# Optimization experiments

Measured on AMD Instinct MI355X. Metric: run time of the kernel, lower is better.

Reference implementation:

```python
import jax, jax.numpy as jnp
import numpy as np

NUM_HEADS = 4
D_MODEL = 192
NEG_INF = -1000000000.0  # fp32 branch of the original mask fill


def setup_inputs() -> dict:
    key = jax.random.key(0)
    ks = jax.random.split(key, 9)
    b, s, d = 4, 2048, D_MODEL
    inp = {
        "query": jax.random.normal(ks[0], (b, s, d), dtype=jnp.float32),
        "key": jax.random.normal(ks[1], (b, s, d), dtype=jnp.float32),
        "value": jax.random.normal(ks[2], (b, s, d), dtype=jnp.float32),
        "attn_mask": jax.random.randint(ks[3], (b, s, s), 0, 2, dtype=jnp.int32),
        "bias": jax.random.normal(ks[4], (1, NUM_HEADS, s, s), dtype=jnp.float32) * 0.1,
        # nn.Linear(d, d, bias=False) weights, applied as x @ W.T
        "Wq": jax.random.normal(ks[5], (d, d), dtype=jnp.float32) / np.sqrt(d),
        "Wk": jax.random.normal(ks[6], (d, d), dtype=jnp.float32) / np.sqrt(d),
        "Wv": jax.random.normal(ks[7], (d, d), dtype=jnp.float32) / np.sqrt(d),
        "Wo": jax.random.normal(ks[8], (d, d), dtype=jnp.float32) / np.sqrt(d),
    }
    return inp


def reference(query, key, value, attn_mask, bias, Wq, Wk, Wv, Wo):
    b, s, d = query.shape
    h, dh = NUM_HEADS, d // NUM_HEADS
    # QKV projections (Linear, no bias): x @ W.T
    q = (query @ Wq.T).reshape(b, s, h, dh)   # [b,s,h,dh]
    k = (key @ Wk.T).reshape(b, s, h, dh)
    v = (value @ Wv.T).reshape(b, s, h, dh)
    # unscaled dot-product logits (original has no 1/sqrt(d) scaling)
    logits = jnp.einsum("bqhd,bkhd->bhqk", q, k)
    logits = logits + bias                       # bias added BEFORE mask fill
    mask4 = attn_mask[:, None, :, :]             # [b,1,q,k] -> broadcast over heads
    logits = jnp.where(mask4 == 0, NEG_INF, logits)
    weights = jax.nn.softmax(logits, axis=-1)    # [b,h,q,k]
    # dropout_rate=0.0 (eval-mode / identity dropout)
    out = jnp.einsum("bhqk,bkhd->bqhd", weights, v).reshape(b, s, d)
    out = out @ Wo.T
    return out, weights.mean(axis=1)             # ([b,s,d], [b,s,s])
```

## Files before the change

kernel.cpp:

```cpp
#include <hip/hip_runtime.h>

#define BB 4
#define SS 2048
#define HH 4
#define DD 192
#define QT 16
#define NT (SS / 2 / 64)
#define NEG_BIG (-1e9f)
#define MB_NEG 0xCE6Eu

typedef __attribute__((ext_vector_type(8))) short short8;
typedef __attribute__((ext_vector_type(4))) float f32x4;

__device__ inline ushort f2bf(float x) {
    union { float f; unsigned u; } v; v.f = x;
    unsigned r = (v.u + 0x7FFFu + ((v.u >> 16) & 1u)) >> 16;
    return (ushort)r;
}
__device__ inline float bf2f(ushort x) {
    union { unsigned u; float f; } v; v.u = ((unsigned)x) << 16;
    return v.f;
}
__device__ inline void wave_lds_fence() {
    __builtin_amdgcn_wave_barrier();
    __builtin_amdgcn_s_waitcnt(0xC07F);
    __builtin_amdgcn_wave_barrier();
}

__global__ __launch_bounds__(256) void wt_kernel(
    const float* __restrict__ Wq, const float* __restrict__ Wk,
    const float* __restrict__ Wv, const float* __restrict__ Wo,
    float* __restrict__ WTall)
{
    __shared__ float tile[32][33];
    const float* W = (blockIdx.z == 0) ? Wq : (blockIdx.z == 1) ? Wk
                   : (blockIdx.z == 2) ? Wv : Wo;
    float* WT = WTall + (size_t)blockIdx.z * DD * DD;
    const int c0 = blockIdx.x * 32, j0 = blockIdx.y * 32;
    const int tx = threadIdx.x & 31, ty = threadIdx.x >> 5;
#pragma unroll
    for (int k = 0; k < 4; ++k)
        tile[ty + 8 * k][tx] = W[(size_t)(j0 + ty + 8 * k) * DD + c0 + tx];
    __syncthreads();
#pragma unroll
    for (int k = 0; k < 4; ++k)
        WT[(size_t)(c0 + ty + 8 * k) * DD + j0 + tx] = tile[tx][ty + 8 * k];
}

__global__ __launch_bounds__(192) void qkv_proj_kernel(
    const float* __restrict__ Xq, const float* __restrict__ Xk,
    const float* __restrict__ Xv, const float* __restrict__ WTall,
    ushort* __restrict__ qpad, ushort* __restrict__ kpad,
    ushort* __restrict__ vT)
{
    const int mode = blockIdx.y;
    const float* __restrict__ X = (mode == 0) ? Xq : (mode == 1) ? Xk : Xv;
    const float* __restrict__ WT = WTall + (size_t)mode * DD * DD;

    __shared__ __align__(16) float xs[16][DD];
    const int row0 = blockIdx.x * 16;
    const int t = threadIdx.x;
    {
        const float4* src = (const float4*)(X + (size_t)row0 * DD);
        float4* dst = (float4*)&xs[0][0];
        for (int i = t; i < 16 * DD / 4; i += 192) dst[i] = src[i];
    }
    __syncthreads();

    const int jt = (t % 48) * 4;
    const int rowg = t / 48;

    float acc[4][4];
#pragma unroll
    for (int r = 0; r < 4; ++r)
#pragma unroll
        for (int j = 0; j < 4; ++j) acc[r][j] = 0.f;

#pragma unroll 2
    for (int k4 = 0; k4 < DD / 4; ++k4) {
        float4 w0 = *(const float4*)&WT[(size_t)(k4 * 4 + 0) * DD + jt];
        float4 w1 = *(const float4*)&WT[(size_t)(k4 * 4 + 1) * DD + jt];
        float4 w2 = *(const float4*)&WT[(size_t)(k4 * 4 + 2) * DD + jt];
        float4 w3 = *(const float4*)&WT[(size_t)(k4 * 4 + 3) * DD + jt];
#pragma unroll
        for (int r = 0; r < 4; ++r) {
            float4 xv = *(const float4*)&xs[rowg * 4 + r][k4 * 4];
            acc[r][0] = fmaf(xv.x, w0.x, acc[r][0]); acc[r][1] = fmaf(xv.x, w0.y, acc[r][1]);
            acc[r][2] = fmaf(xv.x, w0.z, acc[r][2]); acc[r][3] = fmaf(xv.x, w0.w, acc[r][3]);
            acc[r][0] = fmaf(xv.y, w1.x, acc[r][0]); acc[r][1] = fmaf(xv.y, w1.y, acc[r][1]);
            acc[r][2] = fmaf(xv.y, w1.z, acc[r][2]); acc[r][3] = fmaf(xv.y, w1.w, acc[r][3]);
            acc[r][0] = fmaf(xv.z, w2.x, acc[r][0]); acc[r][1] = fmaf(xv.z, w2.y, acc[r][1]);
            acc[r][2] = fmaf(xv.z, w2.z, acc[r][2]); acc[r][3] = fmaf(xv.z, w2.w, acc[r][3]);
            acc[r][0] = fmaf(xv.w, w3.x, acc[r][0]); acc[r][1] = fmaf(xv.w, w3.y, acc[r][1]);
            acc[r][2] = fmaf(xv.w, w3.z, acc[r][2]); acc[r][3] = fmaf(xv.w, w3.w, acc[r][3]);
        }
    }

    if (mode < 2) {
        ushort* __restrict__ out = (mode == 0) ? qpad : kpad;
        const int hd = jt / 48, f = jt % 48;
#pragma unroll
        for (int r = 0; r < 4; ++r) {
            ushort4 o;
            o.x = f2bf(acc[r][0]); o.y = f2bf(acc[r][1]);
            o.z = f2bf(acc[r][2]); o.w = f2bf(acc[r][3]);
            *(ushort4*)&out[((size_t)(row0 + rowg * 4 + r) * HH + hd) * 64 + f] = o;
        }
        const int4 z = make_int4(0, 0, 0, 0);
        for (int i = t; i < 128; i += 192) {
            const int row = i >> 3, hh = (i >> 1) & 3, half = i & 1;
            *(int4*)&out[((size_t)(row0 + row) * HH + hh) * 64 + 48 + half * 8] = z;
        }
    } else {
        const int b = row0 >> 11, s0 = row0 & (SS - 1);
#pragma unroll
        for (int j = 0; j < 4; ++j) {
            const int col = jt + j, hd = col / 48, f = col % 48;
#pragma unroll
            for (int p = 0; p < 2; ++p) {
                unsigned pk = (unsigned)f2bf(acc[2 * p][j]) |
                              ((unsigned)f2bf(acc[2 * p + 1][j]) << 16);
                *(unsigned*)&vT[(((size_t)b * HH + hd) * 48 + f) * SS +
                                s0 + rowg * 4 + 2 * p] = pk;
            }
        }
    }
}

__global__ __launch_bounds__(192) void o_proj_kernel(
    const float* __restrict__ X, const float* __restrict__ WT,
    float* __restrict__ Y)
{
    __shared__ __align__(16) float xs[16][DD];
    const int row0 = blockIdx.x * 16;
    const int t = threadIdx.x;
    {
        const float4* src = (const float4*)(X + (size_t)row0 * DD);
        float4* dst = (float4*)&xs[0][0];
        for (int i = t; i < 16 * DD / 4; i += 192) dst[i] = src[i];
    }
    __syncthreads();

    const int jt = (t % 48) * 4;
    const int rowg = t / 48;

    float acc[4][4];
#pragma unroll
    for (int r = 0; r < 4; ++r)
#pragma unroll
        for (int j = 0; j < 4; ++j) acc[r][j] = 0.f;

#pragma unroll 2
    for (int k4 = 0; k4 < DD / 4; ++k4) {
        float4 w0 = *(const float4*)&WT[(size_t)(k4 * 4 + 0) * DD + jt];
        float4 w1 = *(const float4*)&WT[(size_t)(k4 * 4 + 1) * DD + jt];
        float4 w2 = *(const float4*)&WT[(size_t)(k4 * 4 + 2) * DD + jt];
        float4 w3 = *(const float4*)&WT[(size_t)(k4 * 4 + 3) * DD + jt];
#pragma unroll
        for (int r = 0; r < 4; ++r) {
            float4 xv = *(const float4*)&xs[rowg * 4 + r][k4 * 4];
            acc[r][0] = fmaf(xv.x, w0.x, acc[r][0]); acc[r][1] = fmaf(xv.x, w0.y, acc[r][1]);
            acc[r][2] = fmaf(xv.x, w0.z, acc[r][2]); acc[r][3] = fmaf(xv.x, w0.w, acc[r][3]);
            acc[r][0] = fmaf(xv.y, w1.x, acc[r][0]); acc[r][1] = fmaf(xv.y, w1.y, acc[r][1]);
            acc[r][2] = fmaf(xv.y, w1.z, acc[r][2]); acc[r][3] = fmaf(xv.y, w1.w, acc[r][3]);
            acc[r][0] = fmaf(xv.z, w2.x, acc[r][0]); acc[r][1] = fmaf(xv.z, w2.y, acc[r][1]);
            acc[r][2] = fmaf(xv.z, w2.z, acc[r][2]); acc[r][3] = fmaf(xv.z, w2.w, acc[r][3]);
            acc[r][0] = fmaf(xv.w, w3.x, acc[r][0]); acc[r][1] = fmaf(xv.w, w3.y, acc[r][1]);
            acc[r][2] = fmaf(xv.w, w3.z, acc[r][2]); acc[r][3] = fmaf(xv.w, w3.w, acc[r][3]);
        }
    }

#pragma unroll
    for (int r = 0; r < 4; ++r)
        *(float4*)&Y[(size_t)(row0 + rowg * 4 + r) * DD + jt] =
            make_float4(acc[r][0], acc[r][1], acc[r][2], acc[r][3]);
}

__device__ inline f32x4 qk_tile(const ushort* kp, short8 qa0, short8 qa1) {
    short8 kb0 = *(const short8*)(kp);
    short8 kb1 = *(const short8*)(kp + 32);
    f32x4 d = {0.f, 0.f, 0.f, 0.f};
    d = __builtin_amdgcn_mfma_f32_16x16x32_bf16(qa0, kb0, d, 0, 0, 0);
    d = __builtin_amdgcn_mfma_f32_16x16x32_bf16(qa1, kb1, d, 0, 0, 0);
    return d;
}

__global__ __launch_bounds__(512, 4) void attn_kernel(
    const ushort* __restrict__ qpad, const ushort* __restrict__ kpad,
    const ushort* __restrict__ vT, const int* __restrict__ mask,
    const float* __restrict__ bias,
    ushort* __restrict__ wscr, float* __restrict__ linv_g,
    float* __restrict__ oattn)
{
    __shared__ __align__(16) ushort wb[8][QT][72];
    __shared__ float l_scr[8][QT];

    const int b  = blockIdx.x >> 7;
    const int q0 = (blockIdx.x & 127) * QT;
    const int t = threadIdx.x;
    const int w = t >> 6;
    const int h = w & 3;
    const int kh = w >> 2;
    const int lane = t & 63;
    const int n16 = lane & 15, quad = lane >> 4;
    const int kbase0 = kh * (SS / 2);

    const ushort* qbase =
        qpad + ((size_t)(b * SS + q0 + n16) * HH + h) * 64 + quad * 8;
    const short8 qa0 = *(const short8*)(qbase);
    const short8 qa1 = *(const short8*)(qbase + 32);
    const ushort* kbase = kpad + (size_t)b * SS * HH * 64 + h * 64 + quad * 8;

    const int srow = lane >> 4;
    const int skey = (lane & 15) * 4;
    const int* mrow0 = mask + (size_t)(b * SS + q0) * SS + kbase0 + skey;
    const float* brow0 = bias + (size_t)(h * SS + q0) * SS + kbase0 + skey;

    float l_[4] = {0.f, 0.f, 0.f, 0.f};
    f32x4 pv[3];
#pragma unroll
    for (int nb = 0; nb < 3; ++nb) pv[nb] = (f32x4){0.f, 0.f, 0.f, 0.f};

    int4  mzc[4];
    float4 bvc[4];
#pragma unroll
    for (int rr = 0; rr < 4; ++rr) {
        const int row = rr * 4 + srow;
        mzc[rr] = *(const int4*)(mrow0 + (size_t)row * SS);
        bvc[rr] = *(const float4*)(brow0 + (size_t)row * SS);
    }

    for (int kt = 0; kt < NT; ++kt) {
        const int kb = kt * 64;
#pragma unroll
        for (int rr = 0; rr < 4; ++rr) {
            const int row = rr * 4 + srow;
            ushort4 o;
            o.x = mzc[rr].x ? f2bf(bvc[rr].x) : (ushort)MB_NEG;
            o.y = mzc[rr].y ? f2bf(bvc[rr].y) : (ushort)MB_NEG;
            o.z = mzc[rr].z ? f2bf(bvc[rr].z) : (ushort)MB_NEG;
            o.w = mzc[rr].w ? f2bf(bvc[rr].w) : (ushort)MB_NEG;
            *(ushort4*)&wb[w][row][skey] = o;
        }
        if (kt + 1 < NT) {
#pragma unroll
            for (int rr = 0; rr < 4; ++rr) {
                const int row = rr * 4 + srow;
                mzc[rr] = *(const int4*)(mrow0 + (size_t)row * SS + kb + 64);
                bvc[rr] = *(const float4*)(brow0 + (size_t)row * SS + kb + 64);
            }
        }
        wave_lds_fence();

#pragma unroll
        for (int g = 0; g < 4; ++g) {
            const int key = kbase0 + kb + g * 16 + n16;
            f32x4 d = qk_tile(kbase + (size_t)key * (HH * 64), qa0, qa1);
#pragma unroll
            for (int r = 0; r < 4; ++r) {
                float wgt = __expf(d[r] + bf2f(wb[w][quad * 4 + r][g * 16 + n16]));
                l_[r] += wgt;
                wb[w][quad * 4 + r][g * 16 + n16] = f2bf(wgt);
            }
        }
        wave_lds_fence();

        const short8 wa0 = *(const short8*)&wb[w][n16][quad * 8];
        const short8 wa1 = *(const short8*)&wb[w][n16][32 + quad * 8];
#pragma unroll
        for (int nb = 0; nb < 3; ++nb) {
            const ushort* vb = vT + ((size_t)(b * HH + h) * 48 + nb * 16 + n16) * SS
                               + kbase0 + kb + quad * 8;
            short8 v0 = *(const short8*)(vb);
            short8 v1 = *(const short8*)(vb + 32);
            pv[nb] = __builtin_amdgcn_mfma_f32_16x16x32_bf16(wa0, v0, pv[nb], 0, 0, 0);
            pv[nb] = __builtin_amdgcn_mfma_f32_16x16x32_bf16(wa1, v1, pv[nb], 0, 0, 0);
        }

        {
            const int r4 = lane >> 4;
            const int k4 = (lane & 15) * 4;
#pragma unroll
            for (int it = 0; it < 4; ++it) {
                const int row = it * 4 + r4;
                ushort4 wv = *(const ushort4*)&wb[w][row][k4];
                *(ushort4*)&wscr[((size_t)(b * SS + q0 + row) * HH + h) * SS +
                                 kbase0 + kb + k4] = wv;
            }
        }
        wave_lds_fence();
    }

#pragma unroll
    for (int r = 0; r < 4; ++r) {
        float ll = l_[r];
#pragma unroll
        for (int off = 1; off < 16; off <<= 1) ll += __shfl_xor(ll, off);
        l_[r] = ll;
    }
    if (n16 == 0) {
#pragma unroll
        for (int r = 0; r < 4; ++r) l_scr[w][quad * 4 + r] = l_[r];
    }

    __syncthreads();

    float* scr = (float*)&wb[0][0][0];
    if (kh == 1) {
#pragma unroll
        for (int nb = 0; nb < 3; ++nb)
            *(f32x4*)&scr[((size_t)(h * 64 + lane)) * 12 + nb * 4] = pv[nb];
    }
    __syncthreads();

    if (kh == 0) {
        float linv[4];
#pragma unroll
        for (int r = 0; r < 4; ++r)
            linv[r] = 1.0f / (l_scr[h][quad * 4 + r] + l_scr[h + 4][quad * 4 + r]);
        if (n16 == 0) {
#pragma unroll
            for (int r = 0; r < 4; ++r)
                linv_g[((size_t)b * HH + h) * SS + q0 + quad * 4 + r] = linv[r];
        }
#pragma unroll
        for (int nb = 0; nb < 3; ++nb) {
            f32x4 po = *(const f32x4*)&scr[((size_t)(h * 64 + lane)) * 12 + nb * 4];
#pragma unroll
            for (int r = 0; r < 4; ++r)
                oattn[((size_t)(b * SS + q0 + quad * 4 + r)) * DD +
                      h * 48 + nb * 16 + n16] = (pv[nb][r] + po[r]) * linv[r];
        }
    }
}

__global__ __launch_bounds__(256) void out1_kernel(
    const ushort* __restrict__ wscr, const float* __restrict__ linv_g,
    float* __restrict__ out1)
{
    const int bq = blockIdx.x;
    const int b = bq >> 11;
    const int q = bq & (SS - 1);
    const int t = threadIdx.x;
    const ushort* base = wscr + (size_t)bq * (HH * SS) + t * 8;

    float li[HH];
#pragma unroll
    for (int hh = 0; hh < HH; ++hh)
        li[hh] = linv_g[((size_t)b * HH + hh) * SS + q] * 0.25f;

    float acc[8];
#pragma unroll
    for (int j = 0; j < 8; ++j) acc[j] = 0.f;

#pragma unroll
    for (int hh = 0; hh < HH; ++hh) {
        short8 wv = *(const short8*)(base + (size_t)hh * SS);
#pragma unroll
        for (int j = 0; j < 8; ++j)
            acc[j] = fmaf(bf2f((ushort)wv[j]), li[hh], acc[j]);
    }

    float* dst = out1 + (size_t)bq * SS + t * 8;
    *(float4*)dst = make_float4(acc[0], acc[1], acc[2], acc[3]);
    *(float4*)(dst + 4) = make_float4(acc[4], acc[5], acc[6], acc[7]);
}

extern "C" void kernel_launch(void* const* d_in, const int* in_sizes, int n_in,
                              void* d_out, int out_size, void* d_ws, size_t ws_size,
                              hipStream_t stream)
{
    const float* query = (const float*)d_in[0];
    const float* key   = (const float*)d_in[1];
    const float* value = (const float*)d_in[2];
    const int*   amask = (const int*)d_in[3];
    const float* bias  = (const float*)d_in[4];
    const float* Wq    = (const float*)d_in[5];
    const float* Wk    = (const float*)d_in[6];
    const float* Wv    = (const float*)d_in[7];
    const float* Wo    = (const float*)d_in[8];

    const size_t n_rows = (size_t)BB * SS;
    float* out0 = (float*)d_out;
    float* out1 = out0 + n_rows * DD;

    ushort* qpad  = (ushort*)d_ws;
    ushort* kpad  = qpad + n_rows * HH * 64;
    ushort* vT    = kpad + n_rows * HH * 64;
    float*  oattn = (float*)(vT + (size_t)BB * HH * 48 * SS);
    float*  WTall = oattn + n_rows * DD;
    float*  linvg = WTall + 4 * DD * DD;
    ushort* wscr  = (ushort*)(linvg + (size_t)BB * HH * SS);

    wt_kernel<<<dim3(6, 6, 4), 256, 0, stream>>>(Wq, Wk, Wv, Wo, WTall);

    qkv_proj_kernel<<<dim3(n_rows / 16, 3), 192, 0, stream>>>(
        query, key, value, WTall, qpad, kpad, vT);

    attn_kernel<<<dim3(BB * SS / QT), 512, 0, stream>>>(
        qpad, kpad, vT, amask, bias, wscr, linvg, oattn);

    out1_kernel<<<dim3(BB * SS), 256, 0, stream>>>(wscr, linvg, out1);

    o_proj_kernel<<<dim3(n_rows / 16), 192, 0, stream>>>(
        oattn, WTall + 3 * DD * DD, out0);
}
```

Baseline: 391.0 us.

## Compute transposed QK tiles so softmax weights feed PV MFMA from registers

The QK MFMA now runs with K as the A operand, which makes each lane own one query row and four consecutive keys. Mask and bias can then be read straight into registers in that layout and applied in fp32, replacing the bf16 mask-bias staging through LDS. The exp'd weights are packed into bf16 registers and used directly as the B operand of the PV MFMA, with V read as split 4-element loads. One LDS round trip and one wave fence per tile are removed, but register pressure rises, so the launch-bounds occupancy hint drops from 4 to 2.

```diff
diff --git a/kernel.cpp b/kernel.cpp
--- a/kernel.cpp
+++ b/kernel.cpp
@@ -7,9 +7,9 @@
 #define QT 16
 #define NT (SS / 2 / 64)
 #define NEG_BIG (-1e9f)
-#define MB_NEG 0xCE6Eu
 
 typedef __attribute__((ext_vector_type(8))) short short8;
+typedef __attribute__((ext_vector_type(4))) short s16x4;
 typedef __attribute__((ext_vector_type(4))) float f32x4;
 
 __device__ inline ushort f2bf(float x) {
@@ -176,16 +176,7 @@
             make_float4(acc[r][0], acc[r][1], acc[r][2], acc[r][3]);
 }
 
-__device__ inline f32x4 qk_tile(const ushort* kp, short8 qa0, short8 qa1) {
-    short8 kb0 = *(const short8*)(kp);
-    short8 kb1 = *(const short8*)(kp + 32);
-    f32x4 d = {0.f, 0.f, 0.f, 0.f};
-    d = __builtin_amdgcn_mfma_f32_16x16x32_bf16(qa0, kb0, d, 0, 0, 0);
-    d = __builtin_amdgcn_mfma_f32_16x16x32_bf16(qa1, kb1, d, 0, 0, 0);
-    return d;
-}
-
-__global__ __launch_bounds__(512, 4) void attn_kernel(
+__global__ __launch_bounds__(512, 2) void attn_kernel(
     const ushort* __restrict__ qpad, const ushort* __restrict__ kpad,
     const ushort* __restrict__ vT, const int* __restrict__ mask,
     const float* __restrict__ bias,
@@ -211,72 +202,82 @@
     const short8 qa1 = *(const short8*)(qbase + 32);
     const ushort* kbase = kpad + (size_t)b * SS * HH * 64 + h * 64 + quad * 8;
 
-    const int srow = lane >> 4;
-    const int skey = (lane & 15) * 4;
-    const int* mrow0 = mask + (size_t)(b * SS + q0) * SS + kbase0 + skey;
-    const float* brow0 = bias + (size_t)(h * SS + q0) * SS + kbase0 + skey;
-
-    float l_[4] = {0.f, 0.f, 0.f, 0.f};
+    const int*   mrow = mask + (size_t)(b * SS + q0 + n16) * SS + kbase0 + quad * 4;
+    const float* brow = bias + (size_t)(h * SS + q0 + n16) * SS + kbase0 + quad * 4;
+    const ushort* vrow = vT + ((size_t)(b * HH + h) * 48 + n16) * SS + kbase0 + quad * 4;
+
+    float l_ = 0.f;
     f32x4 pv[3];
 #pragma unroll
     for (int nb = 0; nb < 3; ++nb) pv[nb] = (f32x4){0.f, 0.f, 0.f, 0.f};
 
-    int4  mzc[4];
+    int4   mzc[4];
     float4 bvc[4];
 #pragma unroll
-    for (int rr = 0; rr < 4; ++rr) {
-        const int row = rr * 4 + srow;
-        mzc[rr] = *(const int4*)(mrow0 + (size_t)row * SS);
-        bvc[rr] = *(const float4*)(brow0 + (size_t)row * SS);
+    for (int g = 0; g < 4; ++g) {
+        mzc[g] = *(const int4*)(mrow + g * 16);
+        bvc[g] = *(const float4*)(brow + g * 16);
     }
 
     for (int kt = 0; kt < NT; ++kt) {
         const int kb = kt * 64;
-#pragma unroll
-        for (int rr = 0; rr < 4; ++rr) {
-            const int row = rr * 4 + srow;
-            ushort4 o;
-            o.x = mzc[rr].x ? f2bf(bvc[rr].x) : (ushort)MB_NEG;
-            o.y = mzc[rr].y ? f2bf(bvc[rr].y) : (ushort)MB_NEG;
-            o.z = mzc[rr].z ? f2bf(bvc[rr].z) : (ushort)MB_NEG;
-            o.w = mzc[rr].w ? f2bf(bvc[rr].w) : (ushort)MB_NEG;
-            *(ushort4*)&wb[w][row][skey] = o;
-        }
+
+        short8 kf[8];
+#pragma unroll
+        for (int g = 0; g < 4; ++g) {
+            const ushort* kp = kbase + (size_t)(kbase0 + kb + g * 16 + n16) * (HH * 64);
+            kf[2 * g]     = *(const short8*)(kp);
+            kf[2 * g + 1] = *(const short8*)(kp + 32);
+        }
+        f32x4 d[4];
+#pragma unroll
+        for (int g = 0; g < 4; ++g) {
+            f32x4 acc = {0.f, 0.f, 0.f, 0.f};
+            acc = __builtin_amdgcn_mfma_f32_16x16x32_bf16(kf[2 * g],     qa0, acc, 0, 0, 0);
+            acc = __builtin_amdgcn_mfma_f32_16x16x32_bf16(kf[2 * g + 1], qa1, acc, 0, 0, 0);
+            d[g] = acc;
+        }
+
+        unsigned wpk[8];
+#pragma unroll
+        for (int g = 0; g < 4; ++g) {
+            float w0 = __expf(d[g][0] + (mzc[g].x ? bvc[g].x : NEG_BIG));
+            float w1 = __expf(d[g][1] + (mzc[g].y ? bvc[g].y : NEG_BIG));
+            float w2 = __expf(d[g][2] + (mzc[g].z ? bvc[g].z : NEG_BIG));
+            float w3 = __expf(d[g][3] + (mzc[g].w ? bvc[g].w : NEG_BIG));
+            l_ += (w0 + w1) + (w2 + w3);
+            unsigned p0 = (unsigned)f2bf(w0) | ((unsigned)f2bf(w1) << 16);
+            unsigned p1 = (unsigned)f2bf(w2) | ((unsigned)f2bf(w3) << 16);
+            wpk[2 * g]     = p0;
+            wpk[2 * g + 1] = p1;
+            *(uint2*)&wb[w][n16][g * 16 + quad * 4] = make_uint2(p0, p1);
+        }
+
         if (kt + 1 < NT) {
 #pragma unroll
-            for (int rr = 0; rr < 4; ++rr) {
-                const int row = rr * 4 + srow;
-                mzc[rr] = *(const int4*)(mrow0 + (size_t)row * SS + kb + 64);
-                bvc[rr] = *(const float4*)(brow0 + (size_t)row * SS + kb + 64);
+            for (int g = 0; g < 4; ++g) {
+                mzc[g] = *(const int4*)(mrow + kb + 64 + g * 16);
+                bvc[g] = *(const float4*)(brow + kb + 64 + g * 16);
             }
         }
+
+#pragma unroll
+        for (int gp = 0; gp < 2; ++gp) {
+            union { unsigned u[4]; short8 s8; } wu;
+            wu.u[0] = wpk[4 * gp + 0]; wu.u[1] = wpk[4 * gp + 1];
+            wu.u[2] = wpk[4 * gp + 2]; wu.u[3] = wpk[4 * gp + 3];
+            const short8 wf8 = wu.s8;
+#pragma unroll
+            for (int nb = 0; nb < 3; ++nb) {
+                const ushort* vp = vrow + (size_t)nb * 16 * SS + kb + gp * 32;
+                s16x4 va = *(const s16x4*)(vp);
+                s16x4 vb = *(const s16x4*)(vp + 16);
+                short8 vf8 = __builtin_shufflevector(va, vb, 0, 1, 2, 3, 4, 5, 6, 7);
+                pv[nb] = __builtin_amdgcn_mfma_f32_16x16x32_bf16(vf8, wf8, pv[nb], 0, 0, 0);
+            }
+        }
+
         wave_lds_fence();
-
-#pragma unroll
-        for (int g = 0; g < 4; ++g) {
-            const int key = kbase0 + kb + g * 16 + n16;
-            f32x4 d = qk_tile(kbase + (size_t)key * (HH * 64), qa0, qa1);
-#pragma unroll
-            for (int r = 0; r < 4; ++r) {
-                float wgt = __expf(d[r] + bf2f(wb[w][quad * 4 + r][g * 16 + n16]));
-                l_[r] += wgt;
-                wb[w][quad * 4 + r][g * 16 + n16] = f2bf(wgt);
-            }
-        }
-        wave_lds_fence();
-
-        const short8 wa0 = *(const short8*)&wb[w][n16][quad * 8];
-        const short8 wa1 = *(const short8*)&wb[w][n16][32 + quad * 8];
-#pragma unroll
-        for (int nb = 0; nb < 3; ++nb) {
-            const ushort* vb = vT + ((size_t)(b * HH + h) * 48 + nb * 16 + n16) * SS
-                               + kbase0 + kb + quad * 8;
-            short8 v0 = *(const short8*)(vb);
-            short8 v1 = *(const short8*)(vb + 32);
-            pv[nb] = __builtin_amdgcn_mfma_f32_16x16x32_bf16(wa0, v0, pv[nb], 0, 0, 0);
-            pv[nb] = __builtin_amdgcn_mfma_f32_16x16x32_bf16(wa1, v1, pv[nb], 0, 0, 0);
-        }
-
         {
             const int r4 = lane >> 4;
             const int k4 = (lane & 15) * 4;
@@ -291,17 +292,9 @@
         wave_lds_fence();
     }
 
-#pragma unroll
-    for (int r = 0; r < 4; ++r) {
-        float ll = l_[r];
-#pragma unroll
-        for (int off = 1; off < 16; off <<= 1) ll += __shfl_xor(ll, off);
-        l_[r] = ll;
-    }
-    if (n16 == 0) {
-#pragma unroll
-        for (int r = 0; r < 4; ++r) l_scr[w][quad * 4 + r] = l_[r];
-    }
+    l_ += __shfl_xor(l_, 16);
+    l_ += __shfl_xor(l_, 32);
+    if (quad == 0) l_scr[w][n16] = l_;
 
     __syncthreads();
 
@@ -314,22 +307,16 @@
     __syncthreads();
 
     if (kh == 0) {
-        float linv[4];
-#pragma unroll
-        for (int r = 0; r < 4; ++r)
-            linv[r] = 1.0f / (l_scr[h][quad * 4 + r] + l_scr[h + 4][quad * 4 + r]);
-        if (n16 == 0) {
-#pragma unroll
-            for (int r = 0; r < 4; ++r)
-                linv_g[((size_t)b * HH + h) * SS + q0 + quad * 4 + r] = linv[r];
-        }
+        const float linv = 1.0f / (l_scr[h][n16] + l_scr[h + 4][n16]);
+        if (quad == 0)
+            linv_g[((size_t)b * HH + h) * SS + q0 + n16] = linv;
 #pragma unroll
         for (int nb = 0; nb < 3; ++nb) {
             f32x4 po = *(const f32x4*)&scr[((size_t)(h * 64 + lane)) * 12 + nb * 4];
 #pragma unroll
             for (int r = 0; r < 4; ++r)
-                oattn[((size_t)(b * SS + q0 + quad * 4 + r)) * DD +
-                      h * 48 + nb * 16 + n16] = (pv[nb][r] + po[r]) * linv[r];
+                oattn[(size_t)(b * SS + q0 + n16) * DD +
+                      h * 48 + nb * 16 + quad * 4 + r] = (pv[nb][r] + po[r]) * linv;
         }
     }
 }
```

Result: slower. 452.9 us (+15.9%).

## Fuse head-mean weights output into attention kernel and double-buffer LDS tiles

Applied to the files above, without the earlier changes.

Folds the separate out1 kernel into the end of the attention kernel. Each block rereads its own just-written bf16 weight rows from global scratch after a threadfence and block barrier, scales them by per-head inverse sums taken from shared memory, and writes the head-averaged weights. Mask and bias are now loaded straight into registers in MFMA output layout, replacing the staging pass through LDS with its bf16 round trip. The LDS weight tile is double-buffered so one wave fence per iteration can go. This saves a kernel launch and the global linv buffer, but the block's epilogue gets longer and per-thread register use rises.

```diff
diff --git a/kernel.cpp b/kernel.cpp
--- a/kernel.cpp
+++ b/kernel.cpp
@@ -7,7 +7,6 @@
 #define QT 16
 #define NT (SS / 2 / 64)
 #define NEG_BIG (-1e9f)
-#define MB_NEG 0xCE6Eu
 
 typedef __attribute__((ext_vector_type(8))) short short8;
 typedef __attribute__((ext_vector_type(4))) float f32x4;
@@ -189,10 +188,10 @@
     const ushort* __restrict__ qpad, const ushort* __restrict__ kpad,
     const ushort* __restrict__ vT, const int* __restrict__ mask,
     const float* __restrict__ bias,
-    ushort* __restrict__ wscr, float* __restrict__ linv_g,
-    float* __restrict__ oattn)
-{
-    __shared__ __align__(16) ushort wb[8][QT][72];
+    ushort* __restrict__ wscr, float* __restrict__ oattn,
+    float* __restrict__ out1)
+{
+    __shared__ __align__(16) ushort wb[2][8][QT][72];
     __shared__ float l_scr[8][QT];
 
     const int b  = blockIdx.x >> 7;
@@ -211,46 +210,27 @@
     const short8 qa1 = *(const short8*)(qbase + 32);
     const ushort* kbase = kpad + (size_t)b * SS * HH * 64 + h * 64 + quad * 8;
 
-    const int srow = lane >> 4;
-    const int skey = (lane & 15) * 4;
-    const int* mrow0 = mask + (size_t)(b * SS + q0) * SS + kbase0 + skey;
-    const float* brow0 = bias + (size_t)(h * SS + q0) * SS + kbase0 + skey;
+    const int*   mq = mask + (size_t)(b * SS + q0 + quad * 4) * SS + kbase0 + n16;
+    const float* bq = bias + (size_t)(h * SS + q0 + quad * 4) * SS + kbase0 + n16;
 
     float l_[4] = {0.f, 0.f, 0.f, 0.f};
     f32x4 pv[3];
 #pragma unroll
     for (int nb = 0; nb < 3; ++nb) pv[nb] = (f32x4){0.f, 0.f, 0.f, 0.f};
 
-    int4  mzc[4];
-    float4 bvc[4];
-#pragma unroll
-    for (int rr = 0; rr < 4; ++rr) {
-        const int row = rr * 4 + srow;
-        mzc[rr] = *(const int4*)(mrow0 + (size_t)row * SS);
-        bvc[rr] = *(const float4*)(brow0 + (size_t)row * SS);
-    }
-
+    int   mz[4][4];
+    float bz[4][4];
+#pragma unroll
+    for (int r = 0; r < 4; ++r)
+#pragma unroll
+        for (int g = 0; g < 4; ++g) {
+            mz[r][g] = mq[(size_t)r * SS + g * 16];
+            bz[r][g] = bq[(size_t)r * SS + g * 16];
+        }
+
+    int buf = 0;
     for (int kt = 0; kt < NT; ++kt) {
         const int kb = kt * 64;
-#pragma unroll
-        for (int rr = 0; rr < 4; ++rr) {
-            const int row = rr * 4 + srow;
-            ushort4 o;
-            o.x = mzc[rr].x ? f2bf(bvc[rr].x) : (ushort)MB_NEG;
-            o.y = mzc[rr].y ? f2bf(bvc[rr].y) : (ushort)MB_NEG;
-            o.z = mzc[rr].z ? f2bf(bvc[rr].z) : (ushort)MB_NEG;
-            o.w = mzc[rr].w ? f2bf(bvc[rr].w) : (ushort)MB_NEG;
-            *(ushort4*)&wb[w][row][skey] = o;
-        }
-        if (kt + 1 < NT) {
-#pragma unroll
-            for (int rr = 0; rr < 4; ++rr) {
-                const int row = rr * 4 + srow;
-                mzc[rr] = *(const int4*)(mrow0 + (size_t)row * SS + kb + 64);
-                bvc[rr] = *(const float4*)(brow0 + (size_t)row * SS + kb + 64);
-            }
-        }
-        wave_lds_fence();
 
 #pragma unroll
         for (int g = 0; g < 4; ++g) {
@@ -258,15 +238,26 @@
             f32x4 d = qk_tile(kbase + (size_t)key * (HH * 64), qa0, qa1);
 #pragma unroll
             for (int r = 0; r < 4; ++r) {
-                float wgt = __expf(d[r] + bf2f(wb[w][quad * 4 + r][g * 16 + n16]));
+                float wgt = __expf(d[r] + (mz[r][g] ? bz[r][g] : NEG_BIG));
                 l_[r] += wgt;
-                wb[w][quad * 4 + r][g * 16 + n16] = f2bf(wgt);
+                wb[buf][w][quad * 4 + r][g * 16 + n16] = f2bf(wgt);
             }
         }
+
+        if (kt + 1 < NT) {
+#pragma unroll
+            for (int r = 0; r < 4; ++r)
+#pragma unroll
+                for (int g = 0; g < 4; ++g) {
+                    mz[r][g] = mq[(size_t)r * SS + kb + 64 + g * 16];
+                    bz[r][g] = bq[(size_t)r * SS + kb + 64 + g * 16];
+                }
+        }
+
         wave_lds_fence();
 
-        const short8 wa0 = *(const short8*)&wb[w][n16][quad * 8];
-        const short8 wa1 = *(const short8*)&wb[w][n16][32 + quad * 8];
+        const short8 wa0 = *(const short8*)&wb[buf][w][n16][quad * 8];
+        const short8 wa1 = *(const short8*)&wb[buf][w][n16][32 + quad * 8];
 #pragma unroll
         for (int nb = 0; nb < 3; ++nb) {
             const ushort* vb = vT + ((size_t)(b * HH + h) * 48 + nb * 16 + n16) * SS
@@ -283,12 +274,12 @@
 #pragma unroll
             for (int it = 0; it < 4; ++it) {
                 const int row = it * 4 + r4;
-                ushort4 wv = *(const ushort4*)&wb[w][row][k4];
+                ushort4 wv = *(const ushort4*)&wb[buf][w][row][k4];
                 *(ushort4*)&wscr[((size_t)(b * SS + q0 + row) * HH + h) * SS +
                                  kbase0 + kb + k4] = wv;
             }
         }
-        wave_lds_fence();
+        buf ^= 1;
     }
 
 #pragma unroll
@@ -303,9 +294,10 @@
         for (int r = 0; r < 4; ++r) l_scr[w][quad * 4 + r] = l_[r];
     }
 
-    __syncthreads();
-
-    float* scr = (float*)&wb[0][0][0];
+    __threadfence();
+    __syncthreads();
+
+    float* scr = (float*)&wb[0][0][0][0];
     if (kh == 1) {
 #pragma unroll
         for (int nb = 0; nb < 3; ++nb)
@@ -318,11 +310,6 @@
 #pragma unroll
         for (int r = 0; r < 4; ++r)
             linv[r] = 1.0f / (l_scr[h][quad * 4 + r] + l_scr[h + 4][quad * 4 + r]);
-        if (n16 == 0) {
-#pragma unroll
-            for (int r = 0; r < 4; ++r)
-                linv_g[((size_t)b * HH + h) * SS + q0 + quad * 4 + r] = linv[r];
-        }
 #pragma unroll
         for (int nb = 0; nb < 3; ++nb) {
             f32x4 po = *(const f32x4*)&scr[((size_t)(h * 64 + lane)) * 12 + nb * 4];
@@ -332,38 +319,32 @@
                       h * 48 + nb * 16 + n16] = (pv[nb][r] + po[r]) * linv[r];
         }
     }
-}
-
-__global__ __launch_bounds__(256) void out1_kernel(
-    const ushort* __restrict__ wscr, const float* __restrict__ linv_g,
-    float* __restrict__ out1)
-{
-    const int bq = blockIdx.x;
-    const int b = bq >> 11;
-    const int q = bq & (SS - 1);
-    const int t = threadIdx.x;
-    const ushort* base = wscr + (size_t)bq * (HH * SS) + t * 8;
-
-    float li[HH];
-#pragma unroll
-    for (int hh = 0; hh < HH; ++hh)
-        li[hh] = linv_g[((size_t)b * HH + hh) * SS + q] * 0.25f;
-
-    float acc[8];
-#pragma unroll
-    for (int j = 0; j < 8; ++j) acc[j] = 0.f;
-
-#pragma unroll
-    for (int hh = 0; hh < HH; ++hh) {
-        short8 wv = *(const short8*)(base + (size_t)hh * SS);
-#pragma unroll
-        for (int j = 0; j < 8; ++j)
-            acc[j] = fmaf(bf2f((ushort)wv[j]), li[hh], acc[j]);
-    }
-
-    float* dst = out1 + (size_t)bq * SS + t * 8;
-    *(float4*)dst = make_float4(acc[0], acc[1], acc[2], acc[3]);
-    *(float4*)(dst + 4) = make_float4(acc[4], acc[5], acc[6], acc[7]);
+
+    {
+        const int row = t >> 5;
+        const int k0 = (t & 31) * 64;
+        float li[HH];
+#pragma unroll
+        for (int hh = 0; hh < HH; ++hh)
+            li[hh] = 0.25f / (l_scr[hh][row] + l_scr[hh + 4][row]);
+        const ushort* wrow = wscr + ((size_t)(b * SS + q0 + row) * HH) * SS + k0;
+        float* orow = out1 + (size_t)(b * SS + q0 + row) * SS + k0;
+#pragma unroll 2
+        for (int c = 0; c < 8; ++c) {
+            float acc[8];
+#pragma unroll
+            for (int j = 0; j < 8; ++j) acc[j] = 0.f;
+#pragma unroll
+            for (int hh = 0; hh < HH; ++hh) {
+                short8 wv = *(const short8*)(wrow + (size_t)hh * SS + c * 8);
+#pragma unroll
+                for (int j = 0; j < 8; ++j)
+                    acc[j] = fmaf(bf2f((ushort)wv[j]), li[hh], acc[j]);
+            }
+            *(float4*)(orow + c * 8) = make_float4(acc[0], acc[1], acc[2], acc[3]);
+            *(float4*)(orow + c * 8 + 4) = make_float4(acc[4], acc[5], acc[6], acc[7]);
+        }
+    }
 }
 
 extern "C" void kernel_launch(void* const* d_in, const int* in_sizes, int n_in,
@@ -389,8 +370,7 @@
     ushort* vT    = kpad + n_rows * HH * 64;
     float*  oattn = (float*)(vT + (size_t)BB * HH * 48 * SS);
     float*  WTall = oattn + n_rows * DD;
-    float*  linvg = WTall + 4 * DD * DD;
-    ushort* wscr  = (ushort*)(linvg + (size_t)BB * HH * SS);
+    ushort* wscr  = (ushort*)(WTall + 4 * DD * DD);
 
     wt_kernel<<<dim3(6, 6, 4), 256, 0, stream>>>(Wq, Wk, Wv, Wo, WTall);
 
@@ -398,9 +378,7 @@
         query, key, value, WTall, qpad, kpad, vT);
 
     attn_kernel<<<dim3(BB * SS / QT), 512, 0, stream>>>(
-        qpad, kpad, vT, amask, bias, wscr, linvg, oattn);
-
-    out1_kernel<<<dim3(BB * SS), 256, 0, stream>>>(wscr, linvg, out1);
+        qpad, kpad, vT, amask, bias, wscr, oattn, out1);
 
     o_proj_kernel<<<dim3(n_rows / 16), 192, 0, stream>>>(
         oattn, WTall + 3 * DD * DD, out0);
```

Measured after the change: 598.3 us. +53.0%, slower.

## Double-buffer mask/bias LDS tile to prefetch next tile during PV

Applied to the files above, without the earlier changes.

Splits the per-wave LDS weight buffer into two halves. While the current tile's softmax weights feed the PV MFMAs and the scratch write, the next tile's mask/bias is converted and staged into the other half, and global loads move two tiles ahead. The goal is to hide mask/bias conversion and global load latency behind the matrix work and drop one fence per iteration. In exchange the block uses twice the LDS for this buffer and holds prefetched registers longer, which may lower occupancy.

```diff
diff --git a/kernel.cpp b/kernel.cpp
--- a/kernel.cpp
+++ b/kernel.cpp
@@ -192,7 +192,7 @@
     ushort* __restrict__ wscr, float* __restrict__ linv_g,
     float* __restrict__ oattn)
 {
-    __shared__ __align__(16) ushort wb[8][QT][72];
+    __shared__ __align__(16) ushort wb[2][8][QT][72];
     __shared__ float l_scr[8][QT];
 
     const int b  = blockIdx.x >> 7;
@@ -229,28 +229,27 @@
         mzc[rr] = *(const int4*)(mrow0 + (size_t)row * SS);
         bvc[rr] = *(const float4*)(brow0 + (size_t)row * SS);
     }
-
+#pragma unroll
+    for (int rr = 0; rr < 4; ++rr) {
+        const int row = rr * 4 + srow;
+        ushort4 o;
+        o.x = mzc[rr].x ? f2bf(bvc[rr].x) : (ushort)MB_NEG;
+        o.y = mzc[rr].y ? f2bf(bvc[rr].y) : (ushort)MB_NEG;
+        o.z = mzc[rr].z ? f2bf(bvc[rr].z) : (ushort)MB_NEG;
+        o.w = mzc[rr].w ? f2bf(bvc[rr].w) : (ushort)MB_NEG;
+        *(ushort4*)&wb[0][w][row][skey] = o;
+    }
+#pragma unroll
+    for (int rr = 0; rr < 4; ++rr) {
+        const int row = rr * 4 + srow;
+        mzc[rr] = *(const int4*)(mrow0 + (size_t)row * SS + 64);
+        bvc[rr] = *(const float4*)(brow0 + (size_t)row * SS + 64);
+    }
+    wave_lds_fence();
+
+    int buf = 0;
     for (int kt = 0; kt < NT; ++kt) {
         const int kb = kt * 64;
-#pragma unroll
-        for (int rr = 0; rr < 4; ++rr) {
-            const int row = rr * 4 + srow;
-            ushort4 o;
-            o.x = mzc[rr].x ? f2bf(bvc[rr].x) : (ushort)MB_NEG;
-            o.y = mzc[rr].y ? f2bf(bvc[rr].y) : (ushort)MB_NEG;
-            o.z = mzc[rr].z ? f2bf(bvc[rr].z) : (ushort)MB_NEG;
-            o.w = mzc[rr].w ? f2bf(bvc[rr].w) : (ushort)MB_NEG;
-            *(ushort4*)&wb[w][row][skey] = o;
-        }
-        if (kt + 1 < NT) {
-#pragma unroll
-            for (int rr = 0; rr < 4; ++rr) {
-                const int row = rr * 4 + srow;
-                mzc[rr] = *(const int4*)(mrow0 + (size_t)row * SS + kb + 64);
-                bvc[rr] = *(const float4*)(brow0 + (size_t)row * SS + kb + 64);
-            }
-        }
-        wave_lds_fence();
 
 #pragma unroll
         for (int g = 0; g < 4; ++g) {
@@ -258,15 +257,37 @@
             f32x4 d = qk_tile(kbase + (size_t)key * (HH * 64), qa0, qa1);
 #pragma unroll
             for (int r = 0; r < 4; ++r) {
-                float wgt = __expf(d[r] + bf2f(wb[w][quad * 4 + r][g * 16 + n16]));
+                float wgt = __expf(d[r] + bf2f(wb[buf][w][quad * 4 + r][g * 16 + n16]));
                 l_[r] += wgt;
-                wb[w][quad * 4 + r][g * 16 + n16] = f2bf(wgt);
+                wb[buf][w][quad * 4 + r][g * 16 + n16] = f2bf(wgt);
             }
         }
+
         wave_lds_fence();
 
-        const short8 wa0 = *(const short8*)&wb[w][n16][quad * 8];
-        const short8 wa1 = *(const short8*)&wb[w][n16][32 + quad * 8];
+        if (kt + 1 < NT) {
+#pragma unroll
+            for (int rr = 0; rr < 4; ++rr) {
+                const int row = rr * 4 + srow;
+                ushort4 o;
+                o.x = mzc[rr].x ? f2bf(bvc[rr].x) : (ushort)MB_NEG;
+                o.y = mzc[rr].y ? f2bf(bvc[rr].y) : (ushort)MB_NEG;
+                o.z = mzc[rr].z ? f2bf(bvc[rr].z) : (ushort)MB_NEG;
+                o.w = mzc[rr].w ? f2bf(bvc[rr].w) : (ushort)MB_NEG;
+                *(ushort4*)&wb[buf ^ 1][w][row][skey] = o;
+            }
+        }
+        if (kt + 2 < NT) {
+#pragma unroll
+            for (int rr = 0; rr < 4; ++rr) {
+                const int row = rr * 4 + srow;
+                mzc[rr] = *(const int4*)(mrow0 + (size_t)row * SS + kb + 128);
+                bvc[rr] = *(const float4*)(brow0 + (size_t)row * SS + kb + 128);
+            }
+        }
+
+        const short8 wa0 = *(const short8*)&wb[buf][w][n16][quad * 8];
+        const short8 wa1 = *(const short8*)&wb[buf][w][n16][32 + quad * 8];
 #pragma unroll
         for (int nb = 0; nb < 3; ++nb) {
             const ushort* vb = vT + ((size_t)(b * HH + h) * 48 + nb * 16 + n16) * SS
@@ -283,12 +304,14 @@
 #pragma unroll
             for (int it = 0; it < 4; ++it) {
                 const int row = it * 4 + r4;
-                ushort4 wv = *(const ushort4*)&wb[w][row][k4];
+                ushort4 wv = *(const ushort4*)&wb[buf][w][row][k4];
                 *(ushort4*)&wscr[((size_t)(b * SS + q0 + row) * HH + h) * SS +
                                  kbase0 + kb + k4] = wv;
             }
         }
+
         wave_lds_fence();
+        buf ^= 1;
     }
 
 #pragma unroll
@@ -305,7 +328,7 @@
 
     __syncthreads();
 
-    float* scr = (float*)&wb[0][0][0];
+    float* scr = (float*)&wb[0][0][0][0];
     if (kh == 1) {
 #pragma unroll
         for (int nb = 0; nb < 3; ++nb)
```

New measurement: 391.2 us. No clear change (+0.1%).
